# Performance work log

Hardware: AMD Instinct MI355X
Metric: run time of the kernel (lower is better)

The kernel has to match this reference:

```python
import jax, jax.numpy as jnp
import numpy as np

EPS = 1e-6   # torch pairwise_distance eps added inside the norm
MARGIN = 1.0


def setup_inputs() -> dict:
    key = jax.random.key(0)
    k1, k2 = jax.random.split(key)
    B, K, D = 4096, 1024, 128
    input_features = jax.random.normal(k1, (B, D), dtype=jnp.float32)
    centroids = jax.random.normal(k2, (K, D), dtype=jnp.float32)
    return {"input_features": input_features, "centroids": centroids}


def _mode_rows(idx, num_classes):
    # idx: [B, D] ints in [0, num_classes). Returns per-row mode [B].
    # torch.mode returns the smallest value among ties; jnp.argmax also
    # returns the first (smallest) index among ties, so behavior matches.
    B = idx.shape[0]
    counts = jnp.zeros((B, num_classes), jnp.int32)
    counts = counts.at[jnp.arange(B)[:, None], idx].add(1)
    return jnp.argmax(counts, axis=1)


def reference(input_features, centroids):
    B, D = input_features.shape
    K = centroids.shape[0]

    # [B, K, D] per-dimension squared differences (mse_loss with reduce=False)
    sq = (input_features[:, None, :] - centroids[None, :, :]) ** 2
    idx_min = jnp.argmin(sq, axis=1)  # [B, D] closest centroid per dim
    idx_max = jnp.argmax(sq, axis=1)  # [B, D] furthest centroid per dim

    positives = centroids[_mode_rows(idx_min, K)]  # [B, D]
    negatives = centroids[_mode_rows(idx_max, K)]  # [B, D]

    # triplet_margin_loss(margin=1, p=2, swap=True, reduction='mean');
    # torch adds eps inside the norm: ||a - b + eps||_2
    d_pos = jnp.linalg.norm(input_features - positives + EPS, axis=1)
    d_neg = jnp.linalg.norm(input_features - negatives + EPS, axis=1)
    d_swap = jnp.linalg.norm(positives - negatives + EPS, axis=1)
    d_neg = jnp.minimum(d_neg, d_swap)

    return jnp.mean(jnp.maximum(d_pos - d_neg + MARGIN, 0.0))
```

## Files before the change

### kernel.cpp

```cpp
#include <hip/hip_runtime.h>
#include <cstdint>

#define D 128
#define K 1024
#define NB 4096
#define BB 8
#define TK 64
#define FEPS 1e-6f

typedef unsigned long long u64;
typedef unsigned int u32;
typedef unsigned short u16;


__global__ __launch_bounds__(512) void prep_search_kernel(
    const float* __restrict__ cen, const float* __restrict__ x,
    u16* __restrict__ iminT, float* __restrict__ ext, float* __restrict__ out)
{
    __shared__ u64 keys[K];
    __shared__ u64 skeys[K];
    __shared__ float svs[K];
    __shared__ u16 shs[K];

    const int dcol = blockIdx.x;
    const int t = threadIdx.x;
    if (dcol == 0 && t == 0) out[0] = 0.0f;

    u64 my0, my1;
    {
        float v0 = cen[t * D + dcol];
        float v1 = cen[(t + 512) * D + dcol];
        u32 u0 = __float_as_uint(v0), u1 = __float_as_uint(v1);
        u0 = (u0 & 0x80000000u) ? ~u0 : (u0 | 0x80000000u);
        u1 = (u1 & 0x80000000u) ? ~u1 : (u1 | 0x80000000u);
        my0 = ((u64)u0 << 32) | (u32)t;
        my1 = ((u64)u1 << 32) | (u32)(t + 512);
        keys[t] = my0;
        keys[t + 512] = my1;
    }
    __syncthreads();

    int r0 = 0, r1 = 0;
    #pragma unroll 2
    for (int k0 = 0; k0 < K; k0 += 8) {
        ulonglong2 p0 = *(ulonglong2*)&keys[k0];
        ulonglong2 p1 = *(ulonglong2*)&keys[k0 + 2];
        ulonglong2 p2 = *(ulonglong2*)&keys[k0 + 4];
        ulonglong2 p3 = *(ulonglong2*)&keys[k0 + 6];
        u64 kv[8] = { p0.x, p0.y, p1.x, p1.y, p2.x, p2.y, p3.x, p3.y };
        #pragma unroll
        for (int j = 0; j < 8; ++j) {
            r0 += (kv[j] < my0) ? 1 : 0;
            r1 += (kv[j] < my1) ? 1 : 0;
        }
    }
    skeys[r0] = my0;
    skeys[r1] = my1;
    __syncthreads();

    #pragma unroll
    for (int j = 0; j < 2; ++j) {
        int p = j * 512 + t;
        u64 kp = skeys[p];
        u32 vb = (u32)(kp >> 32);
        int p0 = p;
        while (p0 > 0 && (u32)(skeys[p0 - 1] >> 32) == vb) --p0;
        int head = (int)(skeys[p0] & 1023u);
        u32 u = (vb & 0x80000000u) ? (vb & 0x7FFFFFFFu) : ~vb;
        float v = __uint_as_float(u);
        svs[p] = v;
        shs[p] = (u16)head;
        if (p == 0)     { ext[dcol]     = v; ((int*)ext)[2 * D + dcol] = head; }
        if (p == K - 1) { ext[D + dcol] = v; ((int*)ext)[3 * D + dcol] = head; }
    }
    __syncthreads();

    #pragma unroll 1
    for (int ph = 0; ph < 2; ++ph) {
        const int b0 = ph * 2048;
        float xq[4];
        #pragma unroll
        for (int j = 0; j < 4; ++j)
            xq[j] = x[(size_t)(b0 + j * 512 + t) * D + dcol];

        int pos[4];
        #pragma unroll
        for (int r = 0; r < 4; ++r) pos[r] = -1;
        #pragma unroll
        for (int s = K; s >= 1; s >>= 1) {
            #pragma unroll
            for (int r = 0; r < 4; ++r) {
                int cand = pos[r] + s;
                int cc = cand > K - 1 ? K - 1 : cand;
                float v = svs[cc];
                if (cand <= K - 1 && v <= xq[r]) pos[r] = cand;
            }
        }
        #pragma unroll
        for (int r = 0; r < 4; ++r) {
            int p1 = pos[r], p2 = pos[r] + 1;
            int c1 = p1 < 0 ? 0 : p1;
            int c2 = p2 > K - 1 ? K - 1 : p2;
            float v1 = svs[c1], v2 = svs[c2];
            int h1 = shs[c1], h2 = shs[c2];
            float d1 = xq[r] - v1, d2 = xq[r] - v2;
            float s1 = d1 * d1, s2 = d2 * d2;
            if (p1 < 0) s1 = 3.4e38f;
            if (p2 > K - 1) s2 = 3.4e38f;
            int idx;
            if (s1 < s2) idx = h1;
            else if (s2 < s1) idx = h2;
            else idx = h1 < h2 ? h1 : h2;
            iminT[(size_t)dcol * NB + b0 + r * 512 + t] = (u16)idx;
        }
    }
}

__global__ __launch_bounds__(256) void mode_loss_kernel(
    const float* __restrict__ x, const float* __restrict__ cen,
    const u16* __restrict__ iminT, const float* __restrict__ ext,
    float* __restrict__ out)
{
    __shared__ float xs[BB * D];
    __shared__ u32 cntA[BB * K / 4];
    __shared__ u32 cntB[BB * K / 4];
    __shared__ int modes[2 * BB];

    const int t = threadIdx.x;
    const int b0 = blockIdx.x * BB;

    ((float4*)xs)[t] = ((const float4*)(x + (size_t)b0 * D))[t];
    {
        uint4 z = make_uint4(0u, 0u, 0u, 0u);
        uint4* a4 = (uint4*)cntA;
        uint4* b4 = (uint4*)cntB;
        #pragma unroll
        for (int j = 0; j < 2; ++j) { a4[t + 256 * j] = z; b4[t + 256 * j] = z; }
    }
    __syncthreads();

    {
        const int dd = t >> 1, half = t & 1;
        uint2 w = *(const uint2*)(iminT + (size_t)dd * NB + b0 + half * 4);
        int i0 = (int)(w.x & 0xFFFFu), i1 = (int)(w.x >> 16);
        int i2 = (int)(w.y & 0xFFFFu), i3 = (int)(w.y >> 16);
        const int rr = half * 4;
        atomicAdd(&cntA[((rr + 0) << 8) + (i0 >> 2)], 1u << ((i0 & 3) * 8));
        atomicAdd(&cntA[((rr + 1) << 8) + (i1 >> 2)], 1u << ((i1 & 3) * 8));
        atomicAdd(&cntA[((rr + 2) << 8) + (i2 >> 2)], 1u << ((i2 & 3) * 8));
        atomicAdd(&cntA[((rr + 3) << 8) + (i3 >> 2)], 1u << ((i3 & 3) * 8));
    }

    const int d = t & (D - 1);
    const int g = t >> 7;
    {
        float cminv = ext[d], cmaxv = ext[D + d];
        int cmini = ((const int*)ext)[2 * D + d];
        int cmaxi = ((const int*)ext)[3 * D + d];
        #pragma unroll
        for (int r = 0; r < 4; ++r) {
            float xv = xs[(g * 4 + r) * D + d];
            float d1 = xv - cminv;
            float d2 = xv - cmaxv;
            float s1 = d1 * d1, s2 = d2 * d2;
            int idx;
            if (s1 > s2) idx = cmini;
            else if (s2 > s1) idx = cmaxi;
            else idx = (cmini < cmaxi) ? cmini : cmaxi;
            const int rr = g * 4 + r;
            atomicAdd(&cntB[(rr << 8) + (idx >> 2)], 1u << ((idx & 3) * 8));
        }
    }
    __syncthreads();

    const int row = t >> 5;
    const int lane = t & 31;
    {
        u32 bkeyA = 0u, bkeyB = 0u;
        #pragma unroll
        for (int j = 0; j < 8; ++j) {
            const int w = j * 32 + lane;
            u32 wA = cntA[(row << 8) + w];
            u32 wB = cntB[(row << 8) + w];
            #pragma unroll
            for (int sub = 0; sub < 4; ++sub) {
                const u32 idx = (u32)(w * 4 + sub);
                u32 cA = (wA >> (sub * 8)) & 0xFFu;
                u32 cB = (wB >> (sub * 8)) & 0xFFu;
                u32 kA = (cA << 10) | (1023u - idx);
                u32 kB = (cB << 10) | (1023u - idx);
                bkeyA = kA > bkeyA ? kA : bkeyA;
                bkeyB = kB > bkeyB ? kB : bkeyB;
            }
        }
        #pragma unroll
        for (int m = 16; m >= 1; m >>= 1) {
            u32 oA = __shfl_xor(bkeyA, m);
            u32 oB = __shfl_xor(bkeyB, m);
            bkeyA = oA > bkeyA ? oA : bkeyA;
            bkeyB = oB > bkeyB ? oB : bkeyB;
        }
        if (lane == 0) {
            modes[row]      = 1023 - (int)(bkeyA & 1023u);
            modes[BB + row] = 1023 - (int)(bkeyB & 1023u);
        }
    }
    __syncthreads();

    {
        int pm = modes[row];
        int nm = modes[BB + row];
        const float* pr = cen + (size_t)pm * D;
        const float* nr = cen + (size_t)nm * D;
        float a1 = 0.f, a2 = 0.f, a3 = 0.f;
        #pragma unroll
        for (int j = 0; j < 4; ++j) {
            int dd = j * 32 + lane;
            float xv = xs[row * D + dd];
            float pv = pr[dd], nv = nr[dd];
            float e1 = xv - pv + FEPS;
            float e2 = xv - nv + FEPS;
            float e3 = pv - nv + FEPS;
            a1 += e1 * e1; a2 += e2 * e2; a3 += e3 * e3;
        }
        #pragma unroll
        for (int m = 16; m >= 1; m >>= 1) {
            a1 += __shfl_xor(a1, m);
            a2 += __shfl_xor(a2, m);
            a3 += __shfl_xor(a3, m);
        }
        if (lane == 0) {
            float dp = sqrtf(a1);
            float dneg = fminf(sqrtf(a2), sqrtf(a3));
            float term = dp - dneg + 1.0f;
            if (term > 0.f) atomicAdd(out, term * (1.0f / NB));
        }
    }
}

__global__ __launch_bounds__(256) void col_extremes_kernel(
    const float* __restrict__ cen, float* __restrict__ ws)
{
    __shared__ float mv[256]; __shared__ int mi[256];
    __shared__ float Mv[256]; __shared__ int Mi[256];
    const int dcol = blockIdx.x;
    const int t = threadIdx.x;

    float lminv = 3.4e38f; int lmini = 0;
    float lmaxv = -3.4e38f; int lmaxi = 0;
    #pragma unroll
    for (int j = 0; j < 4; ++j) {
        int k = t * 4 + j;
        float v = cen[k * D + dcol];
        if (v < lminv) { lminv = v; lmini = k; }
        if (v > lmaxv) { lmaxv = v; lmaxi = k; }
    }
    mv[t] = lminv; mi[t] = lmini; Mv[t] = lmaxv; Mi[t] = lmaxi;
    __syncthreads();
    for (int s = 128; s > 0; s >>= 1) {
        if (t < s) {
            float ov = mv[t + s]; int oi = mi[t + s];
            if (ov < mv[t] || (ov == mv[t] && oi < mi[t])) { mv[t] = ov; mi[t] = oi; }
            float Ov = Mv[t + s]; int Oi = Mi[t + s];
            if (Ov > Mv[t] || (Ov == Mv[t] && Oi < Mi[t])) { Mv[t] = Ov; Mi[t] = Oi; }
        }
        __syncthreads();
    }
    if (t == 0) {
        ws[dcol]     = mv[0];
        ws[D + dcol] = Mv[0];
        ((int*)ws)[2 * D + dcol] = mi[0];
        ((int*)ws)[3 * D + dcol] = Mi[0];
    }
}

__global__ __launch_bounds__(256) void cluster_triplet_kernel(
    const float* __restrict__ x, const float* __restrict__ cen,
    const float* __restrict__ ws, float* __restrict__ out)
{
    __shared__ float ctile[TK * D];
    __shared__ float xs[BB * D];
    __shared__ u16 imin[BB * D];
    __shared__ u16 imax[BB * D];
    __shared__ int modes[2 * BB];

    const int t = threadIdx.x;
    const int b0 = blockIdx.x * BB;

    ((float4*)xs)[t] = ((const float4*)(x + (size_t)b0 * D))[t];
    __syncthreads();

    const int d = t & (D - 1);
    const int g = t >> 7;

    float xr[4];
    #pragma unroll
    for (int r = 0; r < 4; ++r) xr[r] = xs[(g * 4 + r) * D + d];

    float best[4]; int bidx[4];
    #pragma unroll
    for (int r = 0; r < 4; ++r) { best[r] = 3.4e38f; bidx[r] = 0; }

    for (int kt = 0; kt < K / TK; ++kt) {
        __syncthreads();
        {
            const float4* src = (const float4*)(cen + (size_t)kt * TK * D);
            float4* dst = (float4*)ctile;
            #pragma unroll
            for (int j = 0; j < 8; ++j) dst[t + 256 * j] = src[t + 256 * j];
        }
        __syncthreads();
        #pragma unroll 8
        for (int kk = 0; kk < TK; ++kk) {
            float cv = ctile[kk * D + d];
            int kg = kt * TK + kk;
            #pragma unroll
            for (int r = 0; r < 4; ++r) {
                float ad = fabsf(xr[r] - cv);
                if (ad < best[r]) { best[r] = ad; bidx[r] = kg; }
            }
        }
    }

    #pragma unroll
    for (int r = 0; r < 4; ++r) imin[(g * 4 + r) * D + d] = (u16)bidx[r];

    {
        float cminv = ws[d], cmaxv = ws[D + d];
        int cmini = ((const int*)ws)[2 * D + d];
        int cmaxi = ((const int*)ws)[3 * D + d];
        #pragma unroll
        for (int r = 0; r < 4; ++r) {
            float d1 = xr[r] - cminv;
            float d2 = xr[r] - cmaxv;
            float s1 = d1 * d1, s2 = d2 * d2;
            int idx;
            if (s1 > s2) idx = cmini;
            else if (s2 > s1) idx = cmaxi;
            else idx = (cmini < cmaxi) ? cmini : cmaxi;
            imax[(g * 4 + r) * D + d] = (u16)idx;
        }
    }
    __syncthreads();

    u32* counts = (u32*)ctile;
    const int row = t >> 5;
    const int lane = t & 31;
    for (int pass = 0; pass < 2; ++pass) {
        {
            uint4* cz = (uint4*)counts;
            uint4 z = make_uint4(0u, 0u, 0u, 0u);
            #pragma unroll
            for (int j = 0; j < 8; ++j) cz[t + 256 * j] = z;
        }
        __syncthreads();
        const u16* src = (pass == 0) ? imin : imax;
        #pragma unroll
        for (int r = 0; r < 4; ++r) {
            int rr = g * 4 + r;
            atomicAdd(&counts[rr * K + (int)src[rr * D + d]], 1u);
        }
        __syncthreads();
        u32 bkey = 0u;
        for (int j = 0; j < 32; ++j) {
            int idx = j * 32 + lane;
            u32 cnt = counts[row * K + idx];
            u32 key = (cnt << 10) | (1023u - (u32)idx);
            bkey = (key > bkey) ? key : bkey;
        }
        #pragma unroll
        for (int m = 16; m >= 1; m >>= 1) {
            u32 o = __shfl_xor(bkey, m);
            bkey = (o > bkey) ? o : bkey;
        }
        if (lane == 0) modes[pass * BB + row] = 1023 - (int)(bkey & 1023u);
        __syncthreads();
    }

    {
        int pm = modes[0 * BB + row];
        int nm = modes[1 * BB + row];
        const float* pr = cen + (size_t)pm * D;
        const float* nr = cen + (size_t)nm * D;
        float a1 = 0.f, a2 = 0.f, a3 = 0.f;
        #pragma unroll
        for (int j = 0; j < 4; ++j) {
            int dd = j * 32 + lane;
            float xv = xs[row * D + dd];
            float pv = pr[dd], nv = nr[dd];
            float e1 = xv - pv + FEPS;
            float e2 = xv - nv + FEPS;
            float e3 = pv - nv + FEPS;
            a1 += e1 * e1; a2 += e2 * e2; a3 += e3 * e3;
        }
        #pragma unroll
        for (int m = 16; m >= 1; m >>= 1) {
            a1 += __shfl_xor(a1, m);
            a2 += __shfl_xor(a2, m);
            a3 += __shfl_xor(a3, m);
        }
        if (lane == 0) {
            float dp = sqrtf(a1);
            float dneg = fminf(sqrtf(a2), sqrtf(a3));
            float term = dp - dneg + 1.0f;
            if (term > 0.f) atomicAdd(out, term * (1.0f / NB));
        }
    }
}

extern "C" void kernel_launch(void* const* d_in, const int* in_sizes, int n_in,
                              void* d_out, int out_size, void* d_ws, size_t ws_size,
                              hipStream_t stream) {
    (void)in_sizes; (void)n_in; (void)out_size;
    const float* x   = (const float*)d_in[0];
    const float* cen = (const float*)d_in[1];
    float* out = (float*)d_out;

    const size_t need = (size_t)D * NB * 2
                      + (size_t)4 * D * 4;
    if (ws_size >= need) {
        u16* iminT  = (u16*)d_ws;
        float* ext  = (float*)(iminT + (size_t)D * NB);
        prep_search_kernel<<<D, 512, 0, stream>>>(cen, x, iminT, ext, out);
        mode_loss_kernel<<<NB / BB, 256, 0, stream>>>(x, cen, iminT, ext, out);
    } else {
        float* ws = (float*)d_ws;
        hipMemsetAsync(d_out, 0, sizeof(float), stream);
        col_extremes_kernel<<<D, 256, 0, stream>>>(cen, ws);
        cluster_triplet_kernel<<<NB / BB, 256, 0, stream>>>(x, cen, ws, out);
    }
}
```

Measured before the change: 114.4 us.

## Replace rank sort and full binary search with 256-bin bucketed sort and search

The O(K) rank-counting sort of each centroid column is replaced by a histogram over 256 value bins, a prefix scan, a scatter into buckets and a rank count within each bucket only. The per-query binary search over all K sorted values is replaced by a bin lookup followed by a binary search inside one bin. This aims to cut shared-memory comparison work in the prep kernel, at the cost of extra barriers, shared atomics and data-dependent loop lengths that diverge within a wavefront.

```diff
diff --git a/kernel.cpp b/kernel.cpp
--- a/kernel.cpp
+++ b/kernel.cpp
@@ -13,49 +13,99 @@
 typedef unsigned short u16;
 
 
+__device__ __forceinline__ int vbin(float v, float vmin, float scale) {
+    float fb = (v - vmin) * scale;
+    fb = fminf(fmaxf(fb, 0.0f), 255.0f);
+    return (int)fb;
+}
+
 __global__ __launch_bounds__(512) void prep_search_kernel(
     const float* __restrict__ cen, const float* __restrict__ x,
     u16* __restrict__ iminT, float* __restrict__ ext, float* __restrict__ out)
 {
-    __shared__ u64 keys[K];
+    __shared__ u64 bkeys[K];
     __shared__ u64 skeys[K];
     __shared__ float svs[K];
     __shared__ u16 shs[K];
+    __shared__ u32 binstart[257];
+    __shared__ u32 pfx[256];
+    __shared__ u32 cursor[256];
+    __shared__ float redmn[8], redmx[8];
 
     const int dcol = blockIdx.x;
     const int t = threadIdx.x;
+    const int wave = t >> 6, lane = t & 63;
     if (dcol == 0 && t == 0) out[0] = 0.0f;
 
-    u64 my0, my1;
-    {
-        float v0 = cen[t * D + dcol];
-        float v1 = cen[(t + 512) * D + dcol];
-        u32 u0 = __float_as_uint(v0), u1 = __float_as_uint(v1);
-        u0 = (u0 & 0x80000000u) ? ~u0 : (u0 | 0x80000000u);
-        u1 = (u1 & 0x80000000u) ? ~u1 : (u1 | 0x80000000u);
-        my0 = ((u64)u0 << 32) | (u32)t;
-        my1 = ((u64)u1 << 32) | (u32)(t + 512);
-        keys[t] = my0;
-        keys[t + 512] = my1;
-    }
-    __syncthreads();
-
-    int r0 = 0, r1 = 0;
-    #pragma unroll 2
-    for (int k0 = 0; k0 < K; k0 += 8) {
-        ulonglong2 p0 = *(ulonglong2*)&keys[k0];
-        ulonglong2 p1 = *(ulonglong2*)&keys[k0 + 2];
-        ulonglong2 p2 = *(ulonglong2*)&keys[k0 + 4];
-        ulonglong2 p3 = *(ulonglong2*)&keys[k0 + 6];
-        u64 kv[8] = { p0.x, p0.y, p1.x, p1.y, p2.x, p2.y, p3.x, p3.y };
-        #pragma unroll
-        for (int j = 0; j < 8; ++j) {
-            r0 += (kv[j] < my0) ? 1 : 0;
-            r1 += (kv[j] < my1) ? 1 : 0;
-        }
-    }
-    skeys[r0] = my0;
-    skeys[r1] = my1;
+    const float v0 = cen[t * D + dcol];
+    const float v1 = cen[(t + 512) * D + dcol];
+
+    float mn = fminf(v0, v1), mx = fmaxf(v0, v1);
+    #pragma unroll
+    for (int s = 32; s >= 1; s >>= 1) {
+        mn = fminf(mn, __shfl_xor(mn, s, 64));
+        mx = fmaxf(mx, __shfl_xor(mx, s, 64));
+    }
+    if (lane == 0) { redmn[wave] = mn; redmx[wave] = mx; }
+    if (t < 257) binstart[t] = 0u;
+    if (t < 256) cursor[t] = 0u;
+    __syncthreads();
+
+    float vmin = redmn[0], vmax = redmx[0];
+    #pragma unroll
+    for (int w = 1; w < 8; ++w) {
+        vmin = fminf(vmin, redmn[w]);
+        vmax = fmaxf(vmax, redmx[w]);
+    }
+    const float range = vmax - vmin;
+    const float scale = (range > 0.0f) ? (255.0f / range) : 0.0f;
+
+    u32 u0 = __float_as_uint(v0), u1 = __float_as_uint(v1);
+    u0 = (u0 & 0x80000000u) ? ~u0 : (u0 | 0x80000000u);
+    u1 = (u1 & 0x80000000u) ? ~u1 : (u1 | 0x80000000u);
+    const u64 k0 = ((u64)u0 << 32) | (u32)t;
+    const u64 k1 = ((u64)u1 << 32) | (u32)(t + 512);
+    const int b0v = vbin(v0, vmin, scale);
+    const int b1v = vbin(v1, vmin, scale);
+    atomicAdd(&binstart[b0v], 1u);
+    atomicAdd(&binstart[b1v], 1u);
+    __syncthreads();
+
+    u32 myh = 0u;
+    if (t < 256) { myh = binstart[t]; pfx[t] = myh; }
+    __syncthreads();
+    #pragma unroll
+    for (int s = 1; s < 256; s <<= 1) {
+        u32 add = 0u;
+        if (t < 256 && t >= s) add = pfx[t - s];
+        __syncthreads();
+        if (t < 256) pfx[t] += add;
+        __syncthreads();
+    }
+    if (t < 256) {
+        u32 st = pfx[t] - myh;
+        binstart[t] = st;
+        cursor[t] = st;
+    }
+    if (t == 0) binstart[256] = K;
+    __syncthreads();
+
+    { u32 s0 = atomicAdd(&cursor[b0v], 1u); bkeys[s0] = k0; }
+    { u32 s1 = atomicAdd(&cursor[b1v], 1u); bkeys[s1] = k1; }
+    __syncthreads();
+
+    {
+        int lo = (int)binstart[b0v], hi = (int)binstart[b0v + 1];
+        int r = lo;
+        for (int p = lo; p < hi; ++p) r += (bkeys[p] < k0) ? 1 : 0;
+        skeys[r] = k0;
+    }
+    {
+        int lo = (int)binstart[b1v], hi = (int)binstart[b1v + 1];
+        int r = lo;
+        for (int p = lo; p < hi; ++p) r += (bkeys[p] < k1) ? 1 : 0;
+        skeys[r] = k1;
+    }
     __syncthreads();
 
     #pragma unroll
@@ -83,27 +133,21 @@
         for (int j = 0; j < 4; ++j)
             xq[j] = x[(size_t)(b0 + j * 512 + t) * D + dcol];
 
-        int pos[4];
-        #pragma unroll
-        for (int r = 0; r < 4; ++r) pos[r] = -1;
-        #pragma unroll
-        for (int s = K; s >= 1; s >>= 1) {
-            #pragma unroll
-            for (int r = 0; r < 4; ++r) {
-                int cand = pos[r] + s;
-                int cc = cand > K - 1 ? K - 1 : cand;
-                float v = svs[cc];
-                if (cand <= K - 1 && v <= xq[r]) pos[r] = cand;
+        #pragma unroll
+        for (int r = 0; r < 4; ++r) {
+            const float xv = xq[r];
+            const int bx = vbin(xv, vmin, scale);
+            int lo = (int)binstart[bx], hi = (int)binstart[bx + 1];
+            while (lo < hi) {
+                int mid = (lo + hi) >> 1;
+                if (svs[mid] <= xv) lo = mid + 1; else hi = mid;
             }
-        }
-        #pragma unroll
-        for (int r = 0; r < 4; ++r) {
-            int p1 = pos[r], p2 = pos[r] + 1;
-            int c1 = p1 < 0 ? 0 : p1;
-            int c2 = p2 > K - 1 ? K - 1 : p2;
-            float v1 = svs[c1], v2 = svs[c2];
+            const int p1 = lo - 1, p2 = lo;
+            const int c1 = p1 < 0 ? 0 : p1;
+            const int c2 = p2 > K - 1 ? K - 1 : p2;
+            float vv1 = svs[c1], vv2 = svs[c2];
             int h1 = shs[c1], h2 = shs[c2];
-            float d1 = xq[r] - v1, d2 = xq[r] - v2;
+            float d1 = xv - vv1, d2 = xv - vv2;
             float s1 = d1 * d1, s2 = d2 * d2;
             if (p1 < 0) s1 = 3.4e38f;
             if (p2 > K - 1) s2 = 3.4e38f;
```

After: 95.57 us. 1.2x faster.
